# Kernel tuning notes

Hardware: AMD Instinct MI355X
Metric: run time of the kernel (lower is better)

Reference implementation:

```python
import jax, jax.numpy as jnp
import numpy as np

B, N, L, S, H, E, D = 4, 32, 256, 256, 8, 64, 64

def setup_inputs() -> dict:
    key = jax.random.key(0)
    k1, k2, k3, k4 = jax.random.split(key, 4)
    queries = jax.random.normal(k1, (B, N, L, H, E), dtype=jnp.float32)
    keys = jax.random.normal(k2, (B, N, S, H, E), dtype=jnp.float32)
    values = jax.random.normal(k3, (B, N, S, H, D), dtype=jnp.float32)
    # additive causal mask [L, S]: 0 where allowed, -1e9 where masked
    causal = jnp.tril(jnp.ones((L, S), dtype=bool))
    attn_mask = jnp.where(causal, 0.0, -1e9).astype(jnp.float32)
    # cross-layer accumulated prior scores [B, N, H, L, S]
    attn_scores = jax.random.normal(k4, (B, N, H, L, S), dtype=jnp.float32) * 0.1
    query_lengths = jnp.full((B,), L, dtype=jnp.int32)
    key_lengths = jnp.full((B,), S, dtype=jnp.int32)
    return {"queries": queries, "keys": keys, "values": values,
            "attn_mask": attn_mask, "attn_scores": attn_scores,
            "query_lengths": query_lengths, "key_lengths": key_lengths}

def reference(queries, keys, values, attn_mask, attn_scores, query_lengths, key_lengths):
    # queries: [B,N,L,H,E], keys: [B,N,S,H,E], values: [B,N,S,H,D]
    e = queries.shape[-1]
    softmax_temp = 1.0 / np.sqrt(e).astype(np.float32)
    QK = jnp.einsum('bnlhe,bnshe->bnhls', queries, keys)
    # additive mask broadcast over [B,N,H]
    scores = QK + attn_mask + attn_scores  # accumulated scores returned for next layer
    A = jax.nn.softmax(softmax_temp * scores, axis=-1)  # dropout omitted (eval mode)
    V = jnp.einsum('bnhls,bnshd->bnlhd', A, values)
    return scores, V
```

## Files before the change

kernel.cpp:

```cpp
#include <hip/hip_runtime.h>
#include <stdint.h>


typedef __attribute__((ext_vector_type(8))) short bfrag;
typedef __attribute__((ext_vector_type(4))) float f32x4;
typedef __attribute__((ext_vector_type(2))) float f32x2;
typedef __attribute__((ext_vector_type(4))) int i32x4;

__device__ __forceinline__ uint32_t f2bf(float f) {
  uint32_t u = __builtin_bit_cast(uint32_t, f);
  return (u + 0x7FFFu + ((u >> 16) & 1u)) >> 16;
}
__device__ __forceinline__ uint32_t pk(float a, float b) {
  return f2bf(a) | (f2bf(b) << 16);
}

#define MFMA(a, b, c) __builtin_amdgcn_mfma_f32_16x16x32_bf16((a), (b), (c), 0, 0, 0)

__global__ __launch_bounds__(1024, 2) void attn_kernel(
    const float* __restrict__ Qg, const float* __restrict__ Kg,
    const float* __restrict__ Vg, const float* __restrict__ Pg,
    float* __restrict__ Sc, float* __restrict__ Ov)
{
  __shared__ char Kb[2][4096];
  __shared__ char Vb[2][4096];

  const int bnh = blockIdx.x;
  const int bn = bnh >> 3, h = bnh & 7;
  const int t = threadIdx.x;
  const int lane = t & 63;
  const int wave = t >> 6;
  const int ql = lane & 15;
  const int g  = lane >> 4;
  const int qt = (int)((0x783C96D25A1EB4F0ull >> (wave * 4)) & 15);
  const int q = qt * 16 + ql;
  const int pvmax = qt >> 1;
  const int swzk = (ql & 7) << 4;
  const int swzv = (ql & 3) << 4;
  const float temp = 0.125f;

  const int kr_ = t >> 5;
  const int kc_ = t & 31;
  const int vd_ = t & 63;
  const int vw_ = t >> 6;
  const float* kgp = Kg + (size_t)bn * 131072 + h * 64 + (size_t)kr_ * 512 + 2 * kc_;
  const float* vgp = Vg + (size_t)bn * 131072 + h * 64 + (size_t)(2 * vw_) * 512 + vd_;
  const int kwoff = (kr_ * 128 + kc_ * 4) ^ ((kr_ & 7) << 4);
  const int vwoff = (vd_ * 64 + vw_ * 4) ^ ((vd_ & 3) << 4);

  f32x2 kreg = *(const f32x2*)kgp;
  float vreg0 = vgp[0], vreg1 = vgp[512];
  *(uint32_t*)(&Kb[0][0] + kwoff) = pk(kreg[0], kreg[1]);
  *(uint32_t*)(&Vb[0][0] + vwoff) = pk(vreg0, vreg1);
  kreg = *(const f32x2*)(kgp + 16384);
  vreg0 = vgp[16384];
  vreg1 = vgp[16384 + 512];

  bfrag qf[2];
#pragma unroll
  for (int ks = 0; ks < 2; ++ks) {
    const float* qp = Qg + (size_t)bn * 131072 + (size_t)q * 512 + h * 64 + ks * 32 + g * 8;
    const f32x4 qa = *(const f32x4*)qp;
    const f32x4 qb = *(const f32x4*)(qp + 4);
    union { i32x4 i; bfrag b; } u;
    u.i = i32x4{(int)pk(qa.x, qa.y), (int)pk(qa.z, qa.w),
                (int)pk(qb.x, qb.y), (int)pk(qb.z, qb.w)};
    qf[ks] = u.b;
  }

  f32x4 O[4];
#pragma unroll
  for (int ds = 0; ds < 4; ++ds) O[ds] = f32x4{0.f, 0.f, 0.f, 0.f};
  float m = -1e30f, lsum = 0.f;

  const size_t scb = (size_t)bnh << 16;
  const float* prp = Pg + scb + (size_t)q * 256 + 4 * g;
  float* scp = Sc + scb + (size_t)q * 256 + 4 * g;

  f32x4 pr0 = __builtin_nontemporal_load((const f32x4*)(prp));
  f32x4 pr1 = __builtin_nontemporal_load((const f32x4*)(prp + 16));

  asm volatile("s_waitcnt lgkmcnt(0)" ::: "memory");
  __builtin_amdgcn_s_barrier();

#pragma unroll 1
  for (int st = 0; st < 8; ++st) {
    const int s0 = st * 32;
    const int p = (st & 1) << 12;
    bfrag kf[2][2];
#pragma unroll
    for (int ss = 0; ss < 2; ++ss)
#pragma unroll
      for (int ks = 0; ks < 2; ++ks)
        kf[ss][ks] = *(const bfrag*)(&Kb[0][0] + p +
            (((16 * ss + ql) * 128 + ks * 64 + g * 16) ^ swzk));

    f32x4 acc[2];
#pragma unroll
    for (int ss = 0; ss < 2; ++ss) {
      f32x4 a = f32x4{0.f, 0.f, 0.f, 0.f};
      a = MFMA(kf[ss][0], qf[0], a);
      a = MFMA(kf[ss][1], qf[1], a);
      const int sb = s0 + 16 * ss + 4 * g;
#pragma unroll
      for (int r = 0; r < 4; ++r)
        a[r] = (sb + r <= q) ? a[r] : a[r] - 1e9f;
      acc[ss] = a + (ss == 0 ? pr0 : pr1);
    }

    if (st < 7) {
      pr0 = __builtin_nontemporal_load((const f32x4*)(prp + (st + 1) * 32));
      pr1 = __builtin_nontemporal_load((const f32x4*)(prp + (st + 1) * 32 + 16));
    }

    __builtin_nontemporal_store(acc[0], (f32x4*)(scp + s0));
    __builtin_nontemporal_store(acc[1], (f32x4*)(scp + s0 + 16));

    if (st <= pvmax) {
      float tm = fmaxf(fmaxf(fmaxf(acc[0][0], acc[0][1]), fmaxf(acc[0][2], acc[0][3])),
                       fmaxf(fmaxf(acc[1][0], acc[1][1]), fmaxf(acc[1][2], acc[1][3])));
      tm = fmaxf(tm, __shfl_xor(tm, 16));
      tm = fmaxf(tm, __shfl_xor(tm, 32));
      tm *= temp;
      const float mnew = fmaxf(m, tm);
      const float fct = __expf(m - mnew);
      m = mnew;
      float pv[8];
#pragma unroll
      for (int ss = 0; ss < 2; ++ss)
#pragma unroll
        for (int r = 0; r < 4; ++r)
          pv[ss * 4 + r] = __expf(fmaf(temp, acc[ss][r], -mnew));
      float ts = (pv[0] + pv[1]) + (pv[2] + pv[3]) + (pv[4] + pv[5]) + (pv[6] + pv[7]);
      ts += __shfl_xor(ts, 16);
      ts += __shfl_xor(ts, 32);
      lsum = lsum * fct + ts;
#pragma unroll
      for (int ds = 0; ds < 4; ++ds) O[ds] *= fct;

      const int w0x = (int)pk(pv[0], pv[1]), w0y = (int)pk(pv[2], pv[3]);
      const int w1x = (int)pk(pv[4], pv[5]), w1y = (int)pk(pv[6], pv[7]);
      const int srcA = ((g & 1) << 5) + ql;
      const int a0 = __shfl(w0x, srcA),      a1 = __shfl(w1x, srcA);
      const int b0 = __shfl(w0y, srcA),      b1 = __shfl(w1y, srcA);
      const int c0 = __shfl(w0x, srcA + 16), c1 = __shfl(w1x, srcA + 16);
      const int d0 = __shfl(w0y, srcA + 16), d1 = __shfl(w1y, srcA + 16);
      union { i32x4 i; bfrag b; } pu;
      pu.i = i32x4{g < 2 ? a0 : a1, g < 2 ? b0 : b1,
                   g < 2 ? c0 : c1, g < 2 ? d0 : d1};

      bfrag vf[4];
#pragma unroll
      for (int ds = 0; ds < 4; ++ds)
        vf[ds] = *(const bfrag*)(&Vb[0][0] + p +
            (((16 * ds + ql) * 64 + g * 16) ^ swzv));
#pragma unroll
      for (int ds = 0; ds < 4; ++ds) O[ds] = MFMA(vf[ds], pu.b, O[ds]);
    }

    if (st < 7) {
      const int p1 = ((st + 1) & 1) << 12;
      *(uint32_t*)(&Kb[0][0] + p1 + kwoff) = pk(kreg[0], kreg[1]);
      *(uint32_t*)(&Vb[0][0] + p1 + vwoff) = pk(vreg0, vreg1);
      if (st < 6) {
        kreg = *(const f32x2*)(kgp + (size_t)(st + 2) * 16384);
        vreg0 = vgp[(st + 2) * 16384];
        vreg1 = vgp[(st + 2) * 16384 + 512];
      }
    }
    asm volatile("s_waitcnt lgkmcnt(0)" ::: "memory");
    __builtin_amdgcn_s_barrier();
  }

  {
    const float inv = 1.f / lsum;
    float* op = Ov + (size_t)bn * 131072 + (size_t)q * 512 + h * 64 + 4 * g;
#pragma unroll
    for (int ds = 0; ds < 4; ++ds) {
      f32x4 o = O[ds] * inv;
      *(f32x4*)(op + 16 * ds) = o;
    }
  }
}

extern "C" void kernel_launch(void* const* d_in, const int* in_sizes, int n_in,
                              void* d_out, int out_size, void* d_ws, size_t ws_size,
                              hipStream_t stream) {
  const float* Qg = (const float*)d_in[0];
  const float* Kg = (const float*)d_in[1];
  const float* Vg = (const float*)d_in[2];
  const float* Pg = (const float*)d_in[4];
  float* Sc = (float*)d_out;
  float* Ov = Sc + (size_t)4 * 32 * 8 * 256 * 256;
  attn_kernel<<<dim3(1024), dim3(1024), 0, stream>>>(Qg, Kg, Vg, Pg, Sc, Ov);
}
```

Baseline: 151.0 us.

## Split each head across two 512-thread blocks by query half, skip unused V tiles

Each (b,n,h) head is now handled by two blocks of 8 waves, each covering half the query rows, instead of one 1024-thread block. Launch bounds change to 512 threads with 6 blocks per CU, aiming for finer scheduling granularity and better occupancy. K/V staging is reworked so each thread loads 4 floats, and the lower-half block skips loading and storing V tiles past the causal limit. K tiles are still loaded redundantly by both blocks, which adds global traffic.

```diff
diff --git a/kernel.cpp b/kernel.cpp
--- a/kernel.cpp
+++ b/kernel.cpp
@@ -4,7 +4,6 @@
 
 typedef __attribute__((ext_vector_type(8))) short bfrag;
 typedef __attribute__((ext_vector_type(4))) float f32x4;
-typedef __attribute__((ext_vector_type(2))) float f32x2;
 typedef __attribute__((ext_vector_type(4))) int i32x4;
 
 __device__ __forceinline__ uint32_t f2bf(float f) {
@@ -17,7 +16,7 @@
 
 #define MFMA(a, b, c) __builtin_amdgcn_mfma_f32_16x16x32_bf16((a), (b), (c), 0, 0, 0)
 
-__global__ __launch_bounds__(1024, 2) void attn_kernel(
+__global__ __launch_bounds__(512, 6) void attn_kernel(
     const float* __restrict__ Qg, const float* __restrict__ Kg,
     const float* __restrict__ Vg, const float* __restrict__ Pg,
     float* __restrict__ Sc, float* __restrict__ Ov)
@@ -25,36 +24,44 @@
   __shared__ char Kb[2][4096];
   __shared__ char Vb[2][4096];
 
-  const int bnh = blockIdx.x;
+  const int b = blockIdx.x;
+  const int bnh  = ((b >> 4) << 3) | (b & 7);
+  const int half = (b >> 3) & 1;
   const int bn = bnh >> 3, h = bnh & 7;
   const int t = threadIdx.x;
   const int lane = t & 63;
   const int wave = t >> 6;
   const int ql = lane & 15;
   const int g  = lane >> 4;
-  const int qt = (int)((0x783C96D25A1EB4F0ull >> (wave * 4)) & 15);
-  const int q = qt * 16 + ql;
-  const int pvmax = qt >> 1;
+  const int qt = (int)((0x54763210u >> (wave * 4)) & 7);
+  const int gqt = half * 8 + qt;
+  const int q = gqt * 16 + ql;
+  const int pvmax = gqt >> 1;
+  const int vmax = half ? 7 : 3;
   const int swzk = (ql & 7) << 4;
   const int swzv = (ql & 3) << 4;
   const float temp = 0.125f;
 
-  const int kr_ = t >> 5;
-  const int kc_ = t & 31;
+  const int kr_ = t >> 4;
+  const int kc4 = (t & 15) * 4;
   const int vd_ = t & 63;
-  const int vw_ = t >> 6;
-  const float* kgp = Kg + (size_t)bn * 131072 + h * 64 + (size_t)kr_ * 512 + 2 * kc_;
-  const float* vgp = Vg + (size_t)bn * 131072 + h * 64 + (size_t)(2 * vw_) * 512 + vd_;
-  const int kwoff = (kr_ * 128 + kc_ * 4) ^ ((kr_ & 7) << 4);
-  const int vwoff = (vd_ * 64 + vw_ * 4) ^ ((vd_ & 3) << 4);
-
-  f32x2 kreg = *(const f32x2*)kgp;
-  float vreg0 = vgp[0], vreg1 = vgp[512];
-  *(uint32_t*)(&Kb[0][0] + kwoff) = pk(kreg[0], kreg[1]);
-  *(uint32_t*)(&Vb[0][0] + vwoff) = pk(vreg0, vreg1);
-  kreg = *(const f32x2*)(kgp + 16384);
-  vreg0 = vgp[16384];
-  vreg1 = vgp[16384 + 512];
+  const int vs4 = (t >> 6) * 4;
+  const float* kgp = Kg + (size_t)bn * 131072 + h * 64 + (size_t)kr_ * 512 + kc4;
+  const float* vgp = Vg + (size_t)bn * 131072 + h * 64 + (size_t)vs4 * 512 + vd_;
+  const int kwoff = (kr_ * 128 + kc4 * 2) ^ ((kr_ & 7) << 4);
+  const int vwoff = (vd_ * 64 + vs4 * 2) ^ ((vd_ & 3) << 4);
+
+  f32x4 kreg = *(const f32x4*)kgp;
+  float vr0 = vgp[0], vr1 = vgp[512], vr2 = vgp[1024], vr3 = vgp[1536];
+  {
+    uint2 kk; kk.x = pk(kreg[0], kreg[1]); kk.y = pk(kreg[2], kreg[3]);
+    *(uint2*)(&Kb[0][0] + kwoff) = kk;
+    uint2 vv; vv.x = pk(vr0, vr1); vv.y = pk(vr2, vr3);
+    *(uint2*)(&Vb[0][0] + vwoff) = vv;
+  }
+  kreg = *(const f32x4*)(kgp + 16384);
+  vr0 = vgp[16384]; vr1 = vgp[16384 + 512];
+  vr2 = vgp[16384 + 1024]; vr3 = vgp[16384 + 1536];
 
   bfrag qf[2];
 #pragma unroll
@@ -160,12 +167,20 @@
 
     if (st < 7) {
       const int p1 = ((st + 1) & 1) << 12;
-      *(uint32_t*)(&Kb[0][0] + p1 + kwoff) = pk(kreg[0], kreg[1]);
-      *(uint32_t*)(&Vb[0][0] + p1 + vwoff) = pk(vreg0, vreg1);
+      uint2 kk; kk.x = pk(kreg[0], kreg[1]); kk.y = pk(kreg[2], kreg[3]);
+      *(uint2*)(&Kb[0][0] + p1 + kwoff) = kk;
+      if (st + 1 <= vmax) {
+        uint2 vv; vv.x = pk(vr0, vr1); vv.y = pk(vr2, vr3);
+        *(uint2*)(&Vb[0][0] + p1 + vwoff) = vv;
+      }
       if (st < 6) {
-        kreg = *(const f32x2*)(kgp + (size_t)(st + 2) * 16384);
-        vreg0 = vgp[(st + 2) * 16384];
-        vreg1 = vgp[(st + 2) * 16384 + 512];
+        kreg = *(const f32x4*)(kgp + (size_t)(st + 2) * 16384);
+        if (st + 2 <= vmax) {
+          vr0 = vgp[(st + 2) * 16384];
+          vr1 = vgp[(st + 2) * 16384 + 512];
+          vr2 = vgp[(st + 2) * 16384 + 1024];
+          vr3 = vgp[(st + 2) * 16384 + 1536];
+        }
       }
     }
     asm volatile("s_waitcnt lgkmcnt(0)" ::: "memory");
@@ -192,5 +207,5 @@
   const float* Pg = (const float*)d_in[4];
   float* Sc = (float*)d_out;
   float* Ov = Sc + (size_t)4 * 32 * 8 * 256 * 256;
-  attn_kernel<<<dim3(1024), dim3(1024), 0, stream>>>(Qg, Kg, Vg, Pg, Sc, Ov);
-}
+  attn_kernel<<<dim3(2048), dim3(512), 0, stream>>>(Qg, Kg, Vg, Pg, Sc, Ov);
+}
```

Result: slower. 225.5 us (+49.3%).
